# Optimization experiments

Measured on AMD Instinct MI355X. Metric: run time of the kernel, lower is better.

Reference implementation:

```python
import jax, jax.numpy as jnp
import numpy as np

B, S, N, F_IN = 4, 256, 500, 32
D, L = 64, 2
TEMP = 0.5
EPS = 1e-5

def gelu(x):
    return jax.nn.gelu(x, approximate=False)  # torch default GELU (erf)

def layernorm(h, g, b):
    mu = h.mean(-1, keepdims=True)
    var = ((h - mu) ** 2).mean(-1, keepdims=True)
    return (h - mu) * jax.lax.rsqrt(var + EPS) * g + b

def gru_last(x_seq, Wih, Whh, bih, bhh):
    # x_seq: [B, T, I]; torch nn.GRU gate math, h0 = 0; returns final hidden [B, D]
    xp = jnp.einsum('bti,gi->btg', x_seq, Wih) + bih  # precompute input gates [B, T, 3D]
    d = Whh.shape[1]
    def step(h, xpt):
        gh = h @ Whh.T + bhh
        xr, xz, xn = jnp.split(xpt, 3, axis=-1)
        hr, hz, hn = jnp.split(gh, 3, axis=-1)
        r = jax.nn.sigmoid(xr + hr)
        z = jax.nn.sigmoid(xz + hz)
        n = jnp.tanh(xn + r * hn)
        return (1.0 - z) * n + z * h, None
    h0 = jnp.zeros((x_seq.shape[0], d), x_seq.dtype)
    h, _ = jax.lax.scan(step, h0, xp.transpose(1, 0, 2))
    return h

def forward(x, ip_W, ip_b, from_embed, to_embed, gl_W, gl_b, gl_g, gl_be,
            Wih_s, Whh_s, bih_s, bhh_s, Wih_m, Whh_m, bih_m, bhh_m,
            Wih_l, Whh_l, bih_l, bhh_l, dh_W1, dh_b1, dh_W2, dh_b2):
    # input_proj: Linear + GELU (Dropout is identity in eval)
    x = gelu(jnp.einsum('bsnf,df->bsnd', x, ip_W) + ip_b)  # [B,S,N,D]
    # learned adjacency: softmax over destination nodes
    adj = jax.nn.softmax((from_embed @ to_embed.T) / TEMP, axis=-1)  # [N,N]
    for i in range(gl_W.shape[0]):
        agg = jnp.einsum('bsnd,nm->bsmd', x, adj)
        h = gelu(jnp.einsum('bsnd,ed->bsne', x + agg, gl_W[i]) + gl_b[i])
        x = layernorm(h, gl_g[i], gl_be[i])
    b, s, n, d = x.shape
    x_flat = x.reshape(b, s, n * d)
    h_s = gru_last(x_flat[:, -10:, :], Wih_s, Whh_s, bih_s, bhh_s)
    h_m = gru_last(x_flat[:, -20:, :], Wih_m, Whh_m, bih_m, bhh_m)
    h_l = gru_last(x_flat, Wih_l, Whh_l, bih_l, bhh_l)
    h = jnp.concatenate([h_s, h_m, h_l], axis=-1)  # [B, 3D]
    h = gelu(h @ dh_W1.T + dh_b1)
    return h @ dh_W2.T + dh_b2  # direction logits [B, N]

def setup_inputs():
    key = jax.random.key(0)
    it = iter(jax.random.split(key, 40))
    rn = lambda shape, s=0.02: jax.random.normal(next(it), shape, jnp.float32) * s
    I = N * D
    return {
        'x': jax.random.normal(next(it), (B, S, N, F_IN), jnp.float32),
        'ip_W': rn((D, F_IN)), 'ip_b': jnp.zeros((D,), jnp.float32),
        'from_embed': rn((N, 32), 0.1), 'to_embed': rn((N, 32), 0.1),
        'gl_W': rn((L, D, D)), 'gl_b': jnp.zeros((L, D), jnp.float32),
        'gl_g': jnp.ones((L, D), jnp.float32), 'gl_be': jnp.zeros((L, D), jnp.float32),
        'Wih_s': rn((3 * D, I)), 'Whh_s': rn((3 * D, D)),
        'bih_s': jnp.zeros((3 * D,), jnp.float32), 'bhh_s': jnp.zeros((3 * D,), jnp.float32),
        'Wih_m': rn((3 * D, I)), 'Whh_m': rn((3 * D, D)),
        'bih_m': jnp.zeros((3 * D,), jnp.float32), 'bhh_m': jnp.zeros((3 * D,), jnp.float32),
        'Wih_l': rn((3 * D, I)), 'Whh_l': rn((3 * D, D)),
        'bih_l': jnp.zeros((3 * D,), jnp.float32), 'bhh_l': jnp.zeros((3 * D,), jnp.float32),
        'dh_W1': rn((D, 3 * D)), 'dh_b1': jnp.zeros((D,), jnp.float32),
        'dh_W2': rn((N, D)), 'dh_b2': jnp.zeros((N,), jnp.float32),
    }

def reference(x, ip_W, ip_b, from_embed, to_embed, gl_W, gl_b, gl_g, gl_be,
              Wih_s, Whh_s, bih_s, bhh_s, Wih_m, Whh_m, bih_m, bhh_m,
              Wih_l, Whh_l, bih_l, bhh_l, dh_W1, dh_b1, dh_W2, dh_b2):
    return forward(x, ip_W, ip_b, from_embed, to_embed, gl_W, gl_b, gl_g, gl_be,
                   Wih_s, Whh_s, bih_s, bhh_s, Wih_m, Whh_m, bih_m, bhh_m,
                   Wih_l, Whh_l, bih_l, bhh_l, dh_W1, dh_b1, dh_W2, dh_b2)
```

## Files before the change

### kernel.cpp

```cpp
#include <hip/hip_runtime.h>
#include <math.h>

#define NN 500
#define DD 64
#define NPAD 512
#define COLS 65536
#define BS_TOT 1024
#define I_DIM 32000
#define KS_GRU 40
#define KSL 800

typedef __attribute__((ext_vector_type(8))) short bf16x8;
typedef __attribute__((ext_vector_type(4))) float f32x4;

__device__ __forceinline__ float gelu_f(float x) {
    return 0.5f * x * (1.0f + erff(x * 0.70710678118654752440f));
}

__device__ __forceinline__ unsigned short bf16_rn(float x) {
    unsigned int u = __float_as_uint(x);
    unsigned int r = u + 0x7FFFu + ((u >> 16) & 1u);
    return (unsigned short)(r >> 16);
}
__device__ __forceinline__ float bf16_tof(unsigned short h) {
    return __uint_as_float(((unsigned int)h) << 16);
}
__device__ __forceinline__ unsigned int pack_hl(float x) {
    unsigned short h = bf16_rn(x);
    unsigned short l = bf16_rn(x - bf16_tof(h));
    return (unsigned int)h | ((unsigned int)l << 16);
}
__device__ __forceinline__ float unpack_val(unsigned int u) {
    return __uint_as_float(u << 16) + __uint_as_float(u & 0xFFFF0000u);
}
__device__ __forceinline__ void split4(float4 v, short4& h4, short4& l4) {
    h4.x = (short)bf16_rn(v.x); l4.x = (short)bf16_rn(v.x - bf16_tof((unsigned short)h4.x));
    h4.y = (short)bf16_rn(v.y); l4.y = (short)bf16_rn(v.y - bf16_tof((unsigned short)h4.y));
    h4.z = (short)bf16_rn(v.z); l4.z = (short)bf16_rn(v.z - bf16_tof((unsigned short)h4.z));
    h4.w = (short)bf16_rn(v.w); l4.w = (short)bf16_rn(v.w - bf16_tof((unsigned short)h4.w));
}

__device__ __forceinline__ int swz_k(int row, int kbyte) {
    return kbyte ^ (((row >> 3) & 3) << 4);
}

__device__ __forceinline__ int frag_off(int row, int q) {
    return ((((row >> 4) * 4 + q) * 16) + (row & 15)) * 16;
}

__global__ __launch_bounds__(512)
void adj_kernel(const float* __restrict__ fe, const float* __restrict__ te,
                short* __restrict__ adjTh, short* __restrict__ adjTl)
{
    __shared__ float fr[32];
    __shared__ float red[8];
    __shared__ float red2[8];
    const int n = blockIdx.x;
    const int tid = threadIdx.x;
    if (tid < 32) fr[tid] = fe[n * 32 + tid];
    __syncthreads();
    const int m = tid;
    float s = -1e30f;
    if (m < NN) {
        float acc = 0.f;
        #pragma unroll
        for (int f = 0; f < 32; ++f) acc += fr[f] * te[m * 32 + f];
        s = acc * 2.0f;
    }
    float v = s;
    #pragma unroll
    for (int off = 32; off; off >>= 1) v = fmaxf(v, __shfl_xor(v, off));
    if ((tid & 63) == 0) red[tid >> 6] = v;
    __syncthreads();
    float bmax = red[0];
    #pragma unroll
    for (int i = 1; i < 8; ++i) bmax = fmaxf(bmax, red[i]);
    float e = (m < NN) ? expf(s - bmax) : 0.f;
    float v2 = e;
    #pragma unroll
    for (int off = 32; off; off >>= 1) v2 += __shfl_xor(v2, off);
    if ((tid & 63) == 0) red2[tid >> 6] = v2;
    __syncthreads();
    float bsum = 0.f;
    #pragma unroll
    for (int i = 0; i < 8; ++i) bsum += red2[i];
    if (m < NN) {
        float p = e / bsum + ((m == n) ? 1.0f : 0.0f);
        unsigned short h = bf16_rn(p);
        adjTh[(size_t)m * NPAD + n] = (short)h;
        adjTl[(size_t)m * NPAD + n] = (short)bf16_rn(p - bf16_tof(h));
    }
}

__global__ __launch_bounds__(256)
void wsplit_kernel(const float* __restrict__ W, short* __restrict__ H,
                   short* __restrict__ L, int n4)
{
    int i = blockIdx.x * 256 + threadIdx.x;
    if (i < n4) {
        float4 v = *(const float4*)&W[i * 4];
        short4 h4, l4;
        split4(v, h4, l4);
        *(short4*)&H[i * 4] = h4;
        *(short4*)&L[i * 4] = l4;
    }
}

__global__ __launch_bounds__(256)
void proj_mfma_kernel(const float* __restrict__ xin,
                      const short* __restrict__ Wh, const short* __restrict__ Wl,
                      const float* __restrict__ ipb, unsigned int* __restrict__ Xhl)
{
    const int tid  = threadIdx.x;
    const int lane = tid & 63;
    const int wave = tid >> 6;
    const int q = lane >> 4, r16 = lane & 15;
    const size_t row0 = (size_t)blockIdx.x * 128 + wave * 32;

    float bB[4];
    #pragma unroll
    for (int ci = 0; ci < 4; ++ci) bB[ci] = ipb[ci * 16 + r16];

    bf16x8 wh[4], wl[4];
    #pragma unroll
    for (int ci = 0; ci < 4; ++ci) {
        int off = (ci * 16 + r16) * 32 + q * 8;
        wh[ci] = *(const bf16x8*)&Wh[off];
        wl[ci] = *(const bf16x8*)&Wl[off];
    }

    f32x4 acc[2][4];
    #pragma unroll
    for (int i = 0; i < 2; ++i)
        #pragma unroll
        for (int j = 0; j < 4; ++j) acc[i][j] = (f32x4){0.f, 0.f, 0.f, 0.f};

    #pragma unroll
    for (int mi = 0; mi < 2; ++mi) {
        const size_t row = row0 + mi * 16 + r16;
        const int n = (int)(row >> 10), bs = (int)(row & 1023);
        const float* src = &xin[((size_t)bs * NN + n) * 32 + q * 8];
        float4 v0 = *(const float4*)src;
        float4 v1 = *(const float4*)(src + 4);
        short4 h0, l0, h1, l1;
        split4(v0, h0, l0);
        split4(v1, h1, l1);
        bf16x8 ah, al;
        ah[0] = h0.x; ah[1] = h0.y; ah[2] = h0.z; ah[3] = h0.w;
        ah[4] = h1.x; ah[5] = h1.y; ah[6] = h1.z; ah[7] = h1.w;
        al[0] = l0.x; al[1] = l0.y; al[2] = l0.z; al[3] = l0.w;
        al[4] = l1.x; al[5] = l1.y; al[6] = l1.z; al[7] = l1.w;
        #pragma unroll
        for (int ci = 0; ci < 4; ++ci) {
            acc[mi][ci] = __builtin_amdgcn_mfma_f32_16x16x32_bf16(ah, wh[ci], acc[mi][ci], 0, 0, 0);
            acc[mi][ci] = __builtin_amdgcn_mfma_f32_16x16x32_bf16(ah, wl[ci], acc[mi][ci], 0, 0, 0);
            acc[mi][ci] = __builtin_amdgcn_mfma_f32_16x16x32_bf16(al, wh[ci], acc[mi][ci], 0, 0, 0);
        }
    }

    #pragma unroll
    for (int mi = 0; mi < 2; ++mi) {
        #pragma unroll
        for (int rg = 0; rg < 4; ++rg) {
            size_t grow = row0 + mi * 16 + q * 4 + rg;
            #pragma unroll
            for (int ci = 0; ci < 4; ++ci) {
                float y = gelu_f(acc[mi][ci][rg] + bB[ci]);
                Xhl[grow * 64 + ci * 16 + r16] = pack_hl(y);
            }
        }
    }
}

__global__ __launch_bounds__(256)
void agg_mfma_kernel(const unsigned int* __restrict__ Xhl,
                     const short* __restrict__ adjTh, const short* __restrict__ adjTl,
                     unsigned int* __restrict__ Yhl)
{
    __shared__ __align__(16) short Ah[2][4096];
    __shared__ __align__(16) short Al[2][4096];
    __shared__ __align__(16) short Bh[2][4096];
    __shared__ __align__(16) short Bl[2][4096];

    const int tid  = threadIdx.x;
    const int lane = tid & 63;
    const int wave = tid >> 6;
    const int wm = (wave >> 1) * 64;
    const int wc = (wave & 1) * 64;
    const int q = lane >> 4, r16 = lane & 15;
    const int m0 = blockIdx.x * 128;
    const int c0 = blockIdx.y * 128;

    const int sa_m = tid >> 1, sa_kh = tid & 1;
    const int sb_c = tid & 127, sb_kh = tid >> 7;
    const size_t cb = (size_t)(c0 + sb_c);

    f32x4 acc[4][4];
    #pragma unroll
    for (int i = 0; i < 4; ++i)
        #pragma unroll
        for (int j = 0; j < 4; ++j) acc[i][j] = (f32x4){0.f, 0.f, 0.f, 0.f};

    {
        const size_t base = (size_t)(m0 + sa_m) * NPAD + sa_kh * 16;
        bf16x8 h0 = *(const bf16x8*)&adjTh[base];
        bf16x8 h1 = *(const bf16x8*)&adjTh[base + 8];
        bf16x8 l0 = *(const bf16x8*)&adjTl[base];
        bf16x8 l1 = *(const bf16x8*)&adjTl[base + 8];
        *(bf16x8*)((char*)Ah[0] + frag_off(sa_m, sa_kh * 2))     = h0;
        *(bf16x8*)((char*)Ah[0] + frag_off(sa_m, sa_kh * 2 + 1)) = h1;
        *(bf16x8*)((char*)Al[0] + frag_off(sa_m, sa_kh * 2))     = l0;
        *(bf16x8*)((char*)Al[0] + frag_off(sa_m, sa_kh * 2 + 1)) = l1;

        unsigned int u[16];
        #pragma unroll
        for (int j = 0; j < 16; ++j) {
            int kk = sb_kh * 16 + j;
            u[j] = (kk < NN) ? Xhl[(size_t)kk * COLS + cb] : 0u;
        }
        bf16x8 bh0, bh1, bl0, bl1;
        #pragma unroll
        for (int j = 0; j < 8; ++j) {
            bh0[j] = (short)(u[j] & 0xFFFFu);     bl0[j] = (short)(u[j] >> 16);
            bh1[j] = (short)(u[8 + j] & 0xFFFFu); bl1[j] = (short)(u[8 + j] >> 16);
        }
        *(bf16x8*)((char*)Bh[0] + frag_off(sb_c, sb_kh * 2))     = bh0;
        *(bf16x8*)((char*)Bh[0] + frag_off(sb_c, sb_kh * 2 + 1)) = bh1;
        *(bf16x8*)((char*)Bl[0] + frag_off(sb_c, sb_kh * 2))     = bl0;
        *(bf16x8*)((char*)Bl[0] + frag_off(sb_c, sb_kh * 2 + 1)) = bl1;
    }
    __syncthreads();

    for (int kc = 0; kc < 16; ++kc) {
        const int cur = kc & 1;
        bf16x8 nAh0, nAh1, nAl0, nAl1;
        unsigned int nu[16];
        if (kc < 15) {
            const int k0n = (kc + 1) * 32;
            const size_t base = (size_t)(m0 + sa_m) * NPAD + k0n + sa_kh * 16;
            nAh0 = *(const bf16x8*)&adjTh[base];
            nAh1 = *(const bf16x8*)&adjTh[base + 8];
            nAl0 = *(const bf16x8*)&adjTl[base];
            nAl1 = *(const bf16x8*)&adjTl[base + 8];
            #pragma unroll
            for (int j = 0; j < 16; ++j) {
                int kk = k0n + sb_kh * 16 + j;
                nu[j] = (kk < NN) ? Xhl[(size_t)kk * COLS + cb] : 0u;
            }
        }
        bf16x8 ah[4], al[4];
        #pragma unroll
        for (int mi = 0; mi < 4; ++mi) {
            int off = frag_off(wm + mi * 16 + r16, q);
            ah[mi] = *(const bf16x8*)((const char*)Ah[cur] + off);
            al[mi] = *(const bf16x8*)((const char*)Al[cur] + off);
        }
        #pragma unroll
        for (int ci = 0; ci < 4; ++ci) {
            int off = frag_off(wc + ci * 16 + r16, q);
            bf16x8 bh = *(const bf16x8*)((const char*)Bh[cur] + off);
            bf16x8 bl = *(const bf16x8*)((const char*)Bl[cur] + off);
            #pragma unroll
            for (int mi = 0; mi < 4; ++mi) {
                acc[mi][ci] = __builtin_amdgcn_mfma_f32_16x16x32_bf16(ah[mi], bh, acc[mi][ci], 0, 0, 0);
                acc[mi][ci] = __builtin_amdgcn_mfma_f32_16x16x32_bf16(ah[mi], bl, acc[mi][ci], 0, 0, 0);
                acc[mi][ci] = __builtin_amdgcn_mfma_f32_16x16x32_bf16(al[mi], bh, acc[mi][ci], 0, 0, 0);
            }
        }
        if (kc < 15) {
            const int nb = cur ^ 1;
            *(bf16x8*)((char*)Ah[nb] + frag_off(sa_m, sa_kh * 2))     = nAh0;
            *(bf16x8*)((char*)Ah[nb] + frag_off(sa_m, sa_kh * 2 + 1)) = nAh1;
            *(bf16x8*)((char*)Al[nb] + frag_off(sa_m, sa_kh * 2))     = nAl0;
            *(bf16x8*)((char*)Al[nb] + frag_off(sa_m, sa_kh * 2 + 1)) = nAl1;
            bf16x8 bh0, bh1, bl0, bl1;
            #pragma unroll
            for (int j = 0; j < 8; ++j) {
                bh0[j] = (short)(nu[j] & 0xFFFFu);     bl0[j] = (short)(nu[j] >> 16);
                bh1[j] = (short)(nu[8 + j] & 0xFFFFu); bl1[j] = (short)(nu[8 + j] >> 16);
            }
            *(bf16x8*)((char*)Bh[nb] + frag_off(sb_c, sb_kh * 2))     = bh0;
            *(bf16x8*)((char*)Bh[nb] + frag_off(sb_c, sb_kh * 2 + 1)) = bh1;
            *(bf16x8*)((char*)Bl[nb] + frag_off(sb_c, sb_kh * 2))     = bl0;
            *(bf16x8*)((char*)Bl[nb] + frag_off(sb_c, sb_kh * 2 + 1)) = bl1;
        }
        __syncthreads();
    }

    #pragma unroll
    for (int mi = 0; mi < 4; ++mi) {
        #pragma unroll
        for (int r = 0; r < 4; ++r) {
            int m = m0 + wm + mi * 16 + q * 4 + r;
            if (m < NN) {
                #pragma unroll
                for (int ci = 0; ci < 4; ++ci) {
                    size_t idx = (size_t)m * COLS + c0 + wc + ci * 16 + r16;
                    Yhl[idx] = pack_hl(acc[mi][ci][r]);
                }
            }
        }
    }
}

__global__ __launch_bounds__(256)
void hln_stream_kernel(unsigned int* __restrict__ Xio,
                       const short* __restrict__ Wh, const short* __restrict__ Wl,
                       const float* __restrict__ glb, const float* __restrict__ glg,
                       const float* __restrict__ glbe)
{
    const int tid  = threadIdx.x;
    const int lane = tid & 63;
    const int wave = tid >> 6;
    const int q = lane >> 4, r16 = lane & 15;
    const size_t row0 = (size_t)blockIdx.x * 128 + wave * 32;

    float bB2[4], bG2[4], bE2[4];
    #pragma unroll
    for (int ci = 0; ci < 4; ++ci) {
        int e = ci * 16 + r16;
        bB2[ci] = glb[e]; bG2[ci] = glg[e]; bE2[ci] = glbe[e];
    }

    f32x4 acc[2][4];
    #pragma unroll
    for (int i = 0; i < 2; ++i)
        #pragma unroll
        for (int j = 0; j < 4; ++j) acc[i][j] = (f32x4){0.f, 0.f, 0.f, 0.f};

    #pragma unroll
    for (int kh = 0; kh < 2; ++kh) {
        bf16x8 wh[4], wl[4];
        #pragma unroll
        for (int ci = 0; ci < 4; ++ci) {
            int off = (ci * 16 + r16) * 64 + kh * 32 + q * 8;
            wh[ci] = *(const bf16x8*)&Wh[off];
            wl[ci] = *(const bf16x8*)&Wl[off];
        }
        #pragma unroll
        for (int mi = 0; mi < 2; ++mi) {
            const size_t row = row0 + mi * 16 + r16;
            const unsigned int* src = &Xio[row * 64 + kh * 32 + q * 8];
            uint4 u0 = *(const uint4*)src;
            uint4 u1 = *(const uint4*)(src + 4);
            bf16x8 ah, al;
            ah[0] = (short)(u0.x & 0xFFFFu); al[0] = (short)(u0.x >> 16);
            ah[1] = (short)(u0.y & 0xFFFFu); al[1] = (short)(u0.y >> 16);
            ah[2] = (short)(u0.z & 0xFFFFu); al[2] = (short)(u0.z >> 16);
            ah[3] = (short)(u0.w & 0xFFFFu); al[3] = (short)(u0.w >> 16);
            ah[4] = (short)(u1.x & 0xFFFFu); al[4] = (short)(u1.x >> 16);
            ah[5] = (short)(u1.y & 0xFFFFu); al[5] = (short)(u1.y >> 16);
            ah[6] = (short)(u1.z & 0xFFFFu); al[6] = (short)(u1.z >> 16);
            ah[7] = (short)(u1.w & 0xFFFFu); al[7] = (short)(u1.w >> 16);
            #pragma unroll
            for (int ci = 0; ci < 4; ++ci) {
                acc[mi][ci] = __builtin_amdgcn_mfma_f32_16x16x32_bf16(ah, wh[ci], acc[mi][ci], 0, 0, 0);
                acc[mi][ci] = __builtin_amdgcn_mfma_f32_16x16x32_bf16(ah, wl[ci], acc[mi][ci], 0, 0, 0);
                acc[mi][ci] = __builtin_amdgcn_mfma_f32_16x16x32_bf16(al, wh[ci], acc[mi][ci], 0, 0, 0);
            }
        }
    }

    #pragma unroll
    for (int mi = 0; mi < 2; ++mi) {
        #pragma unroll
        for (int rg = 0; rg < 4; ++rg) {
            float h[4];
            float s1 = 0.f;
            #pragma unroll
            for (int ci = 0; ci < 4; ++ci) {
                h[ci] = gelu_f(acc[mi][ci][rg] + bB2[ci]);
                s1 += h[ci];
            }
            #pragma unroll
            for (int off = 1; off < 16; off <<= 1) s1 += __shfl_xor(s1, off);
            float mu = s1 * (1.f / 64.f);
            float s2 = 0.f;
            #pragma unroll
            for (int ci = 0; ci < 4; ++ci) { float dc = h[ci] - mu; s2 += dc * dc; }
            #pragma unroll
            for (int off = 1; off < 16; off <<= 1) s2 += __shfl_xor(s2, off);
            float rs = 1.f / sqrtf(s2 * (1.f / 64.f) + 1e-5f);
            size_t grow = row0 + mi * 16 + q * 4 + rg;
            #pragma unroll
            for (int ci = 0; ci < 4; ++ci) {
                float y = (h[ci] - mu) * rs * bG2[ci] + bE2[ci];
                Xio[grow * 64 + ci * 16 + r16] = pack_hl(y);
            }
        }
    }
}

__global__ __launch_bounds__(256)
void wconv_kernel(const float* __restrict__ W0, const float* __restrict__ W1,
                  const float* __restrict__ W2,
                  short* __restrict__ h0, short* __restrict__ l0,
                  short* __restrict__ h1, short* __restrict__ l1,
                  short* __restrict__ h2, short* __restrict__ l2)
{
    const int gi = blockIdx.y;
    const float* W = (gi == 0) ? W0 : (gi == 1) ? W1 : W2;
    short* H = (gi == 0) ? h0 : (gi == 1) ? h1 : h2;
    short* L = (gi == 0) ? l0 : (gi == 1) ? l1 : l2;
    const size_t i = ((size_t)blockIdx.x * 256 + threadIdx.x) * 4;
    float4 v = *(const float4*)&W[i];
    short4 h4, l4;
    split4(v, h4, l4);
    *(short4*)&H[i] = h4;
    *(short4*)&L[i] = l4;
}

__global__ __launch_bounds__(256)
void gru_pre_mfma_kernel(const unsigned int* __restrict__ Xhl,
                         const short* __restrict__ Wh0, const short* __restrict__ Wl0,
                         const short* __restrict__ Wh1, const short* __restrict__ Wl1,
                         const short* __restrict__ Wh2, const short* __restrict__ Wl2,
                         float* __restrict__ p0, float* __restrict__ p1,
                         float* __restrict__ p2)
{
    __shared__ __align__(16) short Ah[64 * 40];
    __shared__ __align__(16) short Al[64 * 40];
    __shared__ __align__(16) short Bh[192 * 40];
    __shared__ __align__(16) short Bl[192 * 40];

    const int bid = blockIdx.x;
    int gi, mtid, ks;
    if (bid < 40)       { gi = 0; mtid = 0;             ks = bid; }
    else if (bid < 120) { int r = bid - 40;  gi = 1; ks = r % 40; mtid = r / 40; }
    else                { int r = bid - 120; gi = 2; ks = r % 40; mtid = r / 40; }
    const short* Wh = (gi == 0) ? Wh0 : (gi == 1) ? Wh1 : Wh2;
    const short* Wl = (gi == 0) ? Wl0 : (gi == 1) ? Wl1 : Wl2;
    float* partial  = (gi == 0) ? p0 : (gi == 1) ? p1 : p2;
    const int Trows = (gi == 0) ? 10 : (gi == 1) ? 20 : 256;
    const int toff  = (gi == 0) ? 246 : (gi == 1) ? 236 : 0;
    const int M     = (gi == 0) ? 40 : (gi == 1) ? 80 : 1024;
    const int R0 = mtid * 64;

    const int tid  = threadIdx.x;
    const int lane = tid & 63;
    const int wave = tid >> 6;
    const int wr = (wave & 1) * 32;
    const int wg = (wave >> 1) * 96;
    const int q = lane >> 4, r16 = lane & 15;

    const int sa_r = tid >> 2, sa_kq = tid & 3;
    const bool vldA = (R0 + sa_r < M);
    int btA = 0;
    if (vldA) { int R = R0 + sa_r; int b = R / Trows, t = R - b * Trows; btA = b * 256 + toff + t; }

    f32x4 acc[2][6];
    #pragma unroll
    for (int i = 0; i < 2; ++i)
        #pragma unroll
        for (int j = 0; j < 6; ++j) acc[i][j] = (f32x4){0.f, 0.f, 0.f, 0.f};

    for (int c = 0; c < KSL / 32; ++c) {
        const int k0 = ks * KSL + c * 32;
        {
            const int kk = k0 + sa_kq * 8;
            const int nn = kk >> 6, d0 = kk & 63;
            uint4 u0 = make_uint4(0u, 0u, 0u, 0u), u1 = u0;
            if (vldA) {
                const unsigned int* src = &Xhl[((size_t)nn * BS_TOT + btA) * 64 + d0];
                u0 = *(const uint4*)src;
                u1 = *(const uint4*)(src + 4);
            }
            short4 h0 = make_short4((short)(u0.x & 0xFFFF), (short)(u0.y & 0xFFFF),
                                    (short)(u0.z & 0xFFFF), (short)(u0.w & 0xFFFF));
            short4 l0 = make_short4((short)(u0.x >> 16), (short)(u0.y >> 16),
                                    (short)(u0.z >> 16), (short)(u0.w >> 16));
            short4 h1 = make_short4((short)(u1.x & 0xFFFF), (short)(u1.y & 0xFFFF),
                                    (short)(u1.z & 0xFFFF), (short)(u1.w & 0xFFFF));
            short4 l1 = make_short4((short)(u1.x >> 16), (short)(u1.y >> 16),
                                    (short)(u1.z >> 16), (short)(u1.w >> 16));
            int kb = swz_k(sa_r, sa_kq * 16);
            char* rowH = (char*)Ah + sa_r * 80;
            char* rowL = (char*)Al + sa_r * 80;
            *(short4*)(rowH + kb) = h0; *(short4*)(rowH + kb + 8) = h1;
            *(short4*)(rowL + kb) = l0; *(short4*)(rowL + kb + 8) = l1;
        }
        #pragma unroll
        for (int l = 0; l < 3; ++l) {
            int idx = tid + l * 256;
            int g = idx >> 2, kq = idx & 3;
            const size_t src = (size_t)g * I_DIM + k0 + kq * 8;
            bf16x8 hv = *(const bf16x8*)&Wh[src];
            bf16x8 lv = *(const bf16x8*)&Wl[src];
            int kb = swz_k(g, kq * 16);
            *(bf16x8*)((char*)Bh + g * 80 + kb) = hv;
            *(bf16x8*)((char*)Bl + g * 80 + kb) = lv;
        }
        __syncthreads();
        bf16x8 ah[2], al[2];
        #pragma unroll
        for (int mi = 0; mi < 2; ++mi) {
            int row = wr + mi * 16 + r16;
            int kb = swz_k(row, q * 16);
            ah[mi] = *(const bf16x8*)((const char*)Ah + row * 80 + kb);
            al[mi] = *(const bf16x8*)((const char*)Al + row * 80 + kb);
        }
        #pragma unroll
        for (int ci = 0; ci < 6; ++ci) {
            int grow = wg + ci * 16 + r16;
            int kb = swz_k(grow, q * 16);
            bf16x8 bh = *(const bf16x8*)((const char*)Bh + grow * 80 + kb);
            bf16x8 bl = *(const bf16x8*)((const char*)Bl + grow * 80 + kb);
            #pragma unroll
            for (int mi = 0; mi < 2; ++mi) {
                acc[mi][ci] = __builtin_amdgcn_mfma_f32_16x16x32_bf16(ah[mi], bh, acc[mi][ci], 0, 0, 0);
                acc[mi][ci] = __builtin_amdgcn_mfma_f32_16x16x32_bf16(ah[mi], bl, acc[mi][ci], 0, 0, 0);
                acc[mi][ci] = __builtin_amdgcn_mfma_f32_16x16x32_bf16(al[mi], bh, acc[mi][ci], 0, 0, 0);
            }
        }
        __syncthreads();
    }
    #pragma unroll
    for (int mi = 0; mi < 2; ++mi) {
        #pragma unroll
        for (int r = 0; r < 4; ++r) {
            int R = R0 + wr + mi * 16 + q * 4 + r;
            if (R < M) {
                #pragma unroll
                for (int ci = 0; ci < 6; ++ci)
                    partial[((size_t)ks * M + R) * 192 + wg + ci * 16 + r16] = acc[mi][ci][r];
            }
        }
    }
}

__global__ __launch_bounds__(192)
void gru_reduce_fused_kernel(const float* __restrict__ p0, const float* __restrict__ p1,
                             const float* __restrict__ p2,
                             const float* __restrict__ bih0, const float* __restrict__ bih1,
                             const float* __restrict__ bih2,
                             float* __restrict__ xp0, float* __restrict__ xp1,
                             float* __restrict__ xp2)
{
    int r = blockIdx.x;
    const float* partial; const float* bih; float* xp; int M;
    if (r < 40)       { partial = p0; bih = bih0; xp = xp0; M = 40; }
    else if (r < 120) { r -= 40;  partial = p1; bih = bih1; xp = xp1; M = 80; }
    else              { r -= 120; partial = p2; bih = bih2; xp = xp2; M = 1024; }
    const int g = threadIdx.x;
    float acc = bih[g];
    for (int ks = 0; ks < KS_GRU; ++ks)
        acc += partial[((size_t)ks * M + r) * 192 + g];
    xp[(size_t)r * 192 + g] = acc;
}

__global__ __launch_bounds__(192)
void gru_scan_kernel(const float* __restrict__ xp_s, const float* __restrict__ xp_m,
                     const float* __restrict__ xp_l,
                     const float* __restrict__ Whh_s, const float* __restrict__ Whh_m,
                     const float* __restrict__ Whh_l,
                     const float* __restrict__ bhh_s, const float* __restrict__ bhh_m,
                     const float* __restrict__ bhh_l,
                     float* __restrict__ hcat)
{
    __shared__ float h[64];
    __shared__ float gh[192];
    const int blk = blockIdx.x;
    const int g3 = blk >> 2, b = blk & 3;
    const float* xp  = (g3 == 0) ? xp_s : (g3 == 1) ? xp_m : xp_l;
    const float* Whh = (g3 == 0) ? Whh_s : (g3 == 1) ? Whh_m : Whh_l;
    const float* bhh = (g3 == 0) ? bhh_s : (g3 == 1) ? bhh_m : bhh_l;
    const int T = (g3 == 0) ? 10 : (g3 == 1) ? 20 : 256;
    const int g = threadIdx.x;

    float w[64];
    #pragma unroll
    for (int k4 = 0; k4 < 16; ++k4) {
        float4 v = *(const float4*)&Whh[g * 64 + k4 * 4];
        w[k4 * 4 + 0] = v.x; w[k4 * 4 + 1] = v.y;
        w[k4 * 4 + 2] = v.z; w[k4 * 4 + 3] = v.w;
    }
    const float bh = bhh[g];
    if (g < 64) h[g] = 0.f;

    const float* xpb = xp + (size_t)b * T * 192;
    float xr_c = 0.f, xz_c = 0.f, xn_c = 0.f;
    if (g < 64) { xr_c = xpb[g]; xz_c = xpb[64 + g]; xn_c = xpb[128 + g]; }
    __syncthreads();

    for (int t = 0; t < T; ++t) {
        float xr_n = 0.f, xz_n = 0.f, xn_n = 0.f;
        if (t + 1 < T && g < 64) {
            const float* xq = xpb + (size_t)(t + 1) * 192;
            xr_n = xq[g]; xz_n = xq[64 + g]; xn_n = xq[128 + g];
        }
        float a0 = 0.f, a1 = 0.f, a2 = 0.f, a3 = 0.f;
        #pragma unroll
        for (int k4 = 0; k4 < 16; ++k4) {
            float4 hv = ((const float4*)h)[k4];
            a0 += hv.x * w[k4 * 4 + 0];
            a1 += hv.y * w[k4 * 4 + 1];
            a2 += hv.z * w[k4 * 4 + 2];
            a3 += hv.w * w[k4 * 4 + 3];
        }
        gh[g] = bh + ((a0 + a1) + (a2 + a3));
        __syncthreads();
        if (g < 64) {
            float hr = gh[g], hz = gh[64 + g], hn = gh[128 + g];
            float r = 1.f / (1.f + __expf(-(xr_c + hr)));
            float z = 1.f / (1.f + __expf(-(xz_c + hz)));
            float pre = xn_c + r * hn;
            float e2 = __expf(2.f * pre);
            float nv = 1.f - 2.f / (e2 + 1.f);
            h[g] = (1.f - z) * nv + z * h[g];
        }
        __syncthreads();
        xr_c = xr_n; xz_c = xz_n; xn_c = xn_n;
    }
    if (g < 64) hcat[b * 192 + g3 * 64 + g] = h[g];
}

__global__ __launch_bounds__(512)
void head_kernel(const float* __restrict__ hcat,
                 const float* __restrict__ W1, const float* __restrict__ b1,
                 const float* __restrict__ W2, const float* __restrict__ b2,
                 float* __restrict__ out)
{
    __shared__ float hc[4][192];
    __shared__ float h1[4][64];
    const int tid = threadIdx.x;
    for (int i = tid; i < 768; i += 512) hc[i / 192][i % 192] = hcat[i];
    __syncthreads();
    if (tid < 256) {
        int b = tid >> 6, e = tid & 63;
        float acc = b1[e];
        #pragma unroll
        for (int k = 0; k < 192; ++k) acc += hc[b][k] * W1[e * 192 + k];
        h1[b][e] = gelu_f(acc);
    }
    __syncthreads();
    for (int o = tid; o < 2000; o += 512) {
        int b = o / 500, n = o % 500;
        float acc = b2[n];
        #pragma unroll
        for (int k = 0; k < 64; ++k) acc += h1[b][k] * W2[n * 64 + k];
        out[o] = acc;
    }
}

extern "C" void kernel_launch(void* const* d_in, const int* in_sizes, int n_in,
                              void* d_out, int out_size, void* d_ws, size_t ws_size,
                              hipStream_t stream)
{
    (void)in_sizes; (void)n_in; (void)out_size; (void)ws_size;
    const float* x    = (const float*)d_in[0];
    const float* ipW  = (const float*)d_in[1];
    const float* ipb  = (const float*)d_in[2];
    const float* fe   = (const float*)d_in[3];
    const float* te   = (const float*)d_in[4];
    const float* glW  = (const float*)d_in[5];
    const float* glb  = (const float*)d_in[6];
    const float* glg  = (const float*)d_in[7];
    const float* glbe = (const float*)d_in[8];
    const float* Wih[3] = {(const float*)d_in[9],  (const float*)d_in[13], (const float*)d_in[17]};
    const float* Whh[3] = {(const float*)d_in[10], (const float*)d_in[14], (const float*)d_in[18]};
    const float* bih[3] = {(const float*)d_in[11], (const float*)d_in[15], (const float*)d_in[19]};
    const float* bhh[3] = {(const float*)d_in[12], (const float*)d_in[16], (const float*)d_in[20]};
    const float* W1 = (const float*)d_in[21];
    const float* b1 = (const float*)d_in[22];
    const float* W2 = (const float*)d_in[23];
    const float* b2 = (const float*)d_in[24];
    float* out = (float*)d_out;

    unsigned int* Xhl = (unsigned int*)d_ws;
    unsigned int* Yhl = Xhl + 32768000;
    short* adjTh = (short*)(Yhl + 32768000);
    short* adjTl = adjTh + NPAD * NPAD;
    short* glWh  = adjTl + NPAD * NPAD;
    short* glWl  = glWh + 8192;
    short* ipWh  = glWl + 8192;
    short* ipWl  = ipWh + 2048;
    short* wbase = (short*)Yhl;
    short* Wh0 = wbase;
    short* Wl0 = Wh0 + 6144000;
    short* Wh1 = Wl0 + 6144000;
    short* Wl1 = Wh1 + 6144000;
    short* Wh2 = Wl1 + 6144000;
    short* Wl2 = Wh2 + 6144000;
    float* pbase = (float*)Yhl + 18432000;
    float* part0 = pbase;
    float* part1 = part0 + 307200;
    float* part2 = part1 + 614400;
    float* xp0   = part2 + 7864320;
    float* xp1   = xp0 + 7680;
    float* xp2   = xp1 + 15360;
    float* hcat  = xp2 + 196608;

    hipMemsetAsync(adjTh, 0, (size_t)NPAD * NPAD * 2 * sizeof(short), stream);
    adj_kernel<<<NN, 512, 0, stream>>>(fe, te, adjTh, adjTl);
    wsplit_kernel<<<8, 256, 0, stream>>>(glW, glWh, glWl, 2048);
    wsplit_kernel<<<2, 256, 0, stream>>>(ipW, ipWh, ipWl, 512);
    proj_mfma_kernel<<<4000, 256, 0, stream>>>(x, ipWh, ipWl, ipb, Xhl);

    agg_mfma_kernel<<<dim3(4, 512), 256, 0, stream>>>(Xhl, adjTh, adjTl, Yhl);
    hln_stream_kernel<<<4000, 256, 0, stream>>>(Yhl, glWh, glWl, glb, glg, glbe);
    agg_mfma_kernel<<<dim3(4, 512), 256, 0, stream>>>(Yhl, adjTh, adjTl, Xhl);
    hln_stream_kernel<<<4000, 256, 0, stream>>>(Xhl, glWh + 4096, glWl + 4096,
                                                glb + 64, glg + 64, glbe + 64);

    wconv_kernel<<<dim3(6000, 3), 256, 0, stream>>>(Wih[0], Wih[1], Wih[2],
                                                    Wh0, Wl0, Wh1, Wl1, Wh2, Wl2);
    gru_pre_mfma_kernel<<<760, 256, 0, stream>>>(Xhl, Wh0, Wl0, Wh1, Wl1, Wh2, Wl2,
                                                 part0, part1, part2);
    gru_reduce_fused_kernel<<<1144, 192, 0, stream>>>(part0, part1, part2,
                                                      bih[0], bih[1], bih[2],
                                                      xp0, xp1, xp2);
    gru_scan_kernel<<<12, 192, 0, stream>>>(xp0, xp1, xp2,
                                            Whh[0], Whh[1], Whh[2],
                                            bhh[0], bhh[1], bhh[2], hcat);
    head_kernel<<<1, 512, 0, stream>>>(hcat, W1, b1, W2, b2, out);
}
```

Before: 727.4 us.

## Run GRU recurrence in a single wavefront without block barriers

The GRU scan kernel shrinks from 192 threads to one 64-thread wavefront. Each thread now holds all three gate rows of Whh in registers and computes its r, z and n gates itself. This removes the shared gate buffer and both __syncthreads per timestep on the serial 256-step chain. In exchange, each thread does three times the FMAs per step and needs about 192 weight registers. The shared h vector is now written and read without a barrier, relying on in-order execution within one wave.

```diff
diff --git a/kernel.cpp b/kernel.cpp
--- a/kernel.cpp
+++ b/kernel.cpp
@@ -548,7 +548,7 @@
     xp[(size_t)r * 192 + g] = acc;
 }
 
-__global__ __launch_bounds__(192)
+__global__ __launch_bounds__(64)
 void gru_scan_kernel(const float* __restrict__ xp_s, const float* __restrict__ xp_m,
                      const float* __restrict__ xp_l,
                      const float* __restrict__ Whh_s, const float* __restrict__ Whh_m,
@@ -558,7 +558,6 @@
                      float* __restrict__ hcat)
 {
     __shared__ float h[64];
-    __shared__ float gh[192];
     const int blk = blockIdx.x;
     const int g3 = blk >> 2, b = blk & 3;
     const float* xp  = (g3 == 0) ? xp_s : (g3 == 1) ? xp_m : xp_l;
@@ -567,51 +566,53 @@
     const int T = (g3 == 0) ? 10 : (g3 == 1) ? 20 : 256;
     const int g = threadIdx.x;
 
-    float w[64];
+    float wr_[64], wz_[64], wn_[64];
     #pragma unroll
     for (int k4 = 0; k4 < 16; ++k4) {
-        float4 v = *(const float4*)&Whh[g * 64 + k4 * 4];
-        w[k4 * 4 + 0] = v.x; w[k4 * 4 + 1] = v.y;
-        w[k4 * 4 + 2] = v.z; w[k4 * 4 + 3] = v.w;
-    }
-    const float bh = bhh[g];
-    if (g < 64) h[g] = 0.f;
+        float4 vr = *(const float4*)&Whh[(size_t)g * 64 + k4 * 4];
+        float4 vz = *(const float4*)&Whh[(size_t)(64 + g) * 64 + k4 * 4];
+        float4 vn = *(const float4*)&Whh[(size_t)(128 + g) * 64 + k4 * 4];
+        wr_[k4 * 4 + 0] = vr.x; wr_[k4 * 4 + 1] = vr.y; wr_[k4 * 4 + 2] = vr.z; wr_[k4 * 4 + 3] = vr.w;
+        wz_[k4 * 4 + 0] = vz.x; wz_[k4 * 4 + 1] = vz.y; wz_[k4 * 4 + 2] = vz.z; wz_[k4 * 4 + 3] = vz.w;
+        wn_[k4 * 4 + 0] = vn.x; wn_[k4 * 4 + 1] = vn.y; wn_[k4 * 4 + 2] = vn.z; wn_[k4 * 4 + 3] = vn.w;
+    }
+    const float bhr = bhh[g], bhz = bhh[64 + g], bhn = bhh[128 + g];
+    h[g] = 0.f;
+    float hown = 0.f;
 
     const float* xpb = xp + (size_t)b * T * 192;
-    float xr_c = 0.f, xz_c = 0.f, xn_c = 0.f;
-    if (g < 64) { xr_c = xpb[g]; xz_c = xpb[64 + g]; xn_c = xpb[128 + g]; }
-    __syncthreads();
+    float xr_c = xpb[g], xz_c = xpb[64 + g], xn_c = xpb[128 + g];
 
     for (int t = 0; t < T; ++t) {
         float xr_n = 0.f, xz_n = 0.f, xn_n = 0.f;
-        if (t + 1 < T && g < 64) {
+        if (t + 1 < T) {
             const float* xq = xpb + (size_t)(t + 1) * 192;
             xr_n = xq[g]; xz_n = xq[64 + g]; xn_n = xq[128 + g];
         }
-        float a0 = 0.f, a1 = 0.f, a2 = 0.f, a3 = 0.f;
+        float ar0 = 0.f, ar1 = 0.f, az0 = 0.f, az1 = 0.f, an0 = 0.f, an1 = 0.f;
         #pragma unroll
         for (int k4 = 0; k4 < 16; ++k4) {
             float4 hv = ((const float4*)h)[k4];
-            a0 += hv.x * w[k4 * 4 + 0];
-            a1 += hv.y * w[k4 * 4 + 1];
-            a2 += hv.z * w[k4 * 4 + 2];
-            a3 += hv.w * w[k4 * 4 + 3];
-        }
-        gh[g] = bh + ((a0 + a1) + (a2 + a3));
-        __syncthreads();
-        if (g < 64) {
-            float hr = gh[g], hz = gh[64 + g], hn = gh[128 + g];
-            float r = 1.f / (1.f + __expf(-(xr_c + hr)));
-            float z = 1.f / (1.f + __expf(-(xz_c + hz)));
-            float pre = xn_c + r * hn;
-            float e2 = __expf(2.f * pre);
-            float nv = 1.f - 2.f / (e2 + 1.f);
-            h[g] = (1.f - z) * nv + z * h[g];
-        }
-        __syncthreads();
+            ar0 += hv.x * wr_[k4 * 4 + 0] + hv.y * wr_[k4 * 4 + 1];
+            ar1 += hv.z * wr_[k4 * 4 + 2] + hv.w * wr_[k4 * 4 + 3];
+            az0 += hv.x * wz_[k4 * 4 + 0] + hv.y * wz_[k4 * 4 + 1];
+            az1 += hv.z * wz_[k4 * 4 + 2] + hv.w * wz_[k4 * 4 + 3];
+            an0 += hv.x * wn_[k4 * 4 + 0] + hv.y * wn_[k4 * 4 + 1];
+            an1 += hv.z * wn_[k4 * 4 + 2] + hv.w * wn_[k4 * 4 + 3];
+        }
+        float hr = bhr + ar0 + ar1;
+        float hz = bhz + az0 + az1;
+        float hn = bhn + an0 + an1;
+        float r = 1.f / (1.f + __expf(-(xr_c + hr)));
+        float z = 1.f / (1.f + __expf(-(xz_c + hz)));
+        float pre = xn_c + r * hn;
+        float e2 = __expf(2.f * pre);
+        float nv = 1.f - 2.f / (e2 + 1.f);
+        hown = (1.f - z) * nv + z * hown;
+        h[g] = hown;
         xr_c = xr_n; xz_c = xz_n; xn_c = xn_n;
     }
-    if (g < 64) hcat[b * 192 + g3 * 64 + g] = h[g];
+    hcat[b * 192 + g3 * 64 + g] = hown;
 }
 
 __global__ __launch_bounds__(512)
@@ -709,8 +710,8 @@
     gru_reduce_fused_kernel<<<1144, 192, 0, stream>>>(part0, part1, part2,
                                                       bih[0], bih[1], bih[2],
                                                       xp0, xp1, xp2);
-    gru_scan_kernel<<<12, 192, 0, stream>>>(xp0, xp1, xp2,
-                                            Whh[0], Whh[1], Whh[2],
-                                            bhh[0], bhh[1], bhh[2], hcat);
+    gru_scan_kernel<<<12, 64, 0, stream>>>(xp0, xp1, xp2,
+                                           Whh[0], Whh[1], Whh[2],
+                                           bhh[0], bhh[1], bhh[2], hcat);
     head_kernel<<<1, 512, 0, stream>>>(hcat, W1, b1, W2, b2, out);
 }
```

Measured after the change: 828.1 us. 13.8% more time.
